# Performance work log

Hardware: AMD Instinct MI355X
Metric: run time of the kernel (lower is better)

## Reference

```python
import jax, jax.numpy as jnp
import numpy as np

D_MODEL = 1024
NUM_HEADS = 16
HEAD_DIM = D_MODEL // NUM_HEADS


def setup_inputs() -> dict:
    key = jax.random.key(0)
    ks = jax.random.split(key, 8)
    B, L, D = 4, 4096, D_MODEL
    s = 1.0 / np.sqrt(D)
    return {
        "x": jax.random.normal(ks[0], (B, L, D), dtype=jnp.float32),
        "y": jax.random.normal(ks[1], (B, L, D), dtype=jnp.float32),
        "Wkv": jax.random.normal(ks[2], (D, 2 * D), dtype=jnp.float32) * s,
        "bkv": jnp.zeros((2 * D,), dtype=jnp.float32),
        "Wq": jax.random.normal(ks[3], (D, D), dtype=jnp.float32) * s,
        "bq": jnp.zeros((D,), dtype=jnp.float32),
        "Wo": jax.random.normal(ks[4], (D, D), dtype=jnp.float32) * s,
        "bo": jnp.zeros((D,), dtype=jnp.float32),
    }


def reference(x, y, Wkv, bkv, Wq, bq, Wo, bo):
    B, L, D = x.shape
    H, hd = NUM_HEADS, HEAD_DIM
    # projections (torch Linear: x @ W^T + b; here W stored as [in,out])
    kv = (x @ Wkv + bkv).reshape(B, L, H, 2 * hd)
    q = (y @ Wq + bq).reshape(B, L, H, hd)
    # NOTE: source's permute() results are discarded, so attention is taken
    # over the HEADS axis at each position: attn shape [B, L, H, H].
    k, v = jnp.split(kv, 2, axis=-1)  # each [B, L, H, hd]
    scale = 1.0 / np.sqrt(hd)
    attn = jnp.einsum("blhd,blgd->blhg", q, k) * scale  # [B,L,H,H]
    attn = jax.nn.softmax(attn, axis=-1)
    val = jnp.einsum("blhg,blgd->blhd", attn, v).reshape(B, L, D)
    return val @ Wo + bo
```

## Files before the change

### kernel.cpp

```cpp
#include <hip/hip_runtime.h>
#include <math.h>


typedef __attribute__((ext_vector_type(8))) short bf16x8;
typedef __attribute__((ext_vector_type(4))) float f32x4;

__device__ __forceinline__ float b2f(short s) {
    union { unsigned u; float f; } x;
    x.u = ((unsigned)(unsigned short)s) << 16;
    return x.f;
}
__device__ __forceinline__ short f2b(float f) {
    union { float f; unsigned u; } x;
    x.f = f;
    unsigned r = (x.u + 0x7FFFu + ((x.u >> 16) & 1u)) >> 16;
    return (short)r;
}

__global__ __launch_bounds__(256) void cast2_f32_bf16(
    const float* __restrict__ in0, short* __restrict__ out0,
    const float* __restrict__ in1, short* __restrict__ out1, int n) {
    int i = (blockIdx.x * 256 + threadIdx.x) * 4;
    const float* in = in0;
    short* out = out0;
    if (i >= n) {
        i -= n;
        in = in1;
        out = out1;
    }
    float4 v = *(const float4*)(in + i);
    short4 o;
    o.x = f2b(v.x); o.y = f2b(v.y); o.z = f2b(v.z); o.w = f2b(v.w);
    *(short4*)(out + i) = o;
}

__global__ __launch_bounds__(256) void transpose_cast2(
    const float* __restrict__ W0, short* __restrict__ Wt0,
    const float* __restrict__ W1, short* __restrict__ Wt1, int K, int N) {
    const float* W = blockIdx.z ? W1 : W0;
    short* Wt = blockIdx.z ? Wt1 : Wt0;
    __shared__ float tile[32][33];
    int tx = threadIdx.x;
    int ty = threadIdx.y;
    int bx = blockIdx.x * 32;
    int by = blockIdx.y * 32;
#pragma unroll
    for (int j = 0; j < 32; j += 8)
        tile[ty + j][tx] = W[(size_t)(by + ty + j) * N + bx + tx];
    __syncthreads();
#pragma unroll
    for (int j = 0; j < 32; j += 8)
        Wt[(size_t)(bx + ty + j) * K + by + tx] = f2b(tile[tx][ty + j]);
}

#define BM 256
#define BN 256
#define BK 64

#define SUBOFF(c, ab, ks) (((((c) * 2 + (ab)) * 2 + (ks))) * 8192)

#define GLD16(g, l)                                           \
    __builtin_amdgcn_global_load_lds(                         \
        (const __attribute__((address_space(1))) void*)(g),   \
        (__attribute__((address_space(3))) void*)(l), 16, 0, 0)

#define STAGE_A(c, ks, kk)                                                   \
    do {                                                                     \
        GLD16(agp + (kk) + (ks) * 32, lbase + SUBOFF(c, 0, ks) * 2 + dst);   \
        GLD16(agp + (kk) + (ks) * 32 + qstep,                                \
              lbase + SUBOFF(c, 0, ks) * 2 + 8192 + dst);                    \
    } while (0)

#define STAGE_B(c, ks, kk)                                                   \
    do {                                                                     \
        GLD16(bgp + (kk) + (ks) * 32, lbase + SUBOFF(c, 1, ks) * 2 + dst);   \
        GLD16(bgp + (kk) + (ks) * 32 + qstep,                                \
              lbase + SUBOFF(c, 1, ks) * 2 + 8192 + dst);                    \
    } while (0)

#define MFMA_CLUSTER(MH)                                                     \
    do {                                                                     \
        asm volatile("s_waitcnt lgkmcnt(0)" ::: "memory");                   \
        __builtin_amdgcn_sched_barrier(0);                                   \
        __builtin_amdgcn_s_setprio(1);                                       \
        _Pragma("unroll") for (int i_ = 0; i_ < 4; ++i_)                     \
            _Pragma("unroll") for (int j_ = 0; j_ < 4; ++j_)                 \
                acc[(MH) + i_][j_] = __builtin_amdgcn_mfma_f32_16x16x32_bf16(\
                    af[i_], bf[j_], acc[(MH) + i_][j_], 0, 0, 0);            \
        __builtin_amdgcn_s_setprio(0);                                       \
    } while (0)

template <int OUT_BF16>
__global__ __launch_bounds__(512, 2) void gemm_bt(
    const short* __restrict__ A,
    const short* __restrict__ Bt,
    const float* __restrict__ bias,
    void* __restrict__ Cout,
    int M, int N, int K) {
    __shared__ __align__(16) short lds[65536];

    const int tid = threadIdx.x;

    const int NX = gridDim.x;
    const int nwg = NX * gridDim.y;
    int lin = blockIdx.y * NX + blockIdx.x;
    lin = (lin & 7) * (nwg >> 3) + (lin >> 3);
    const int bn = (lin % NX) * BN;
    const int bm = (lin / NX) * BM;

    const int lane = tid & 63;
    const int wave = tid >> 6;
    const int wr = wave >> 2;
    const int wc = wave & 3;
    const int fr = lane & 15;
    const int kq = lane >> 4;
    const int rsw = (kq ^ ((fr >> 1) & 3)) << 3;
    const int aro = (wr * 128 + fr) * 32 + rsw;
    const int bro = (wc * 64 + fr) * 32 + rsw;

    const int srow = tid >> 2;
    const int sslot = ((tid & 3) ^ ((tid >> 3) & 3)) * 8;
    const short* agp = A + (size_t)(bm + srow) * K + sslot;
    const short* bgp = Bt + (size_t)(bn + srow) * K + sslot;
    const size_t qstep = (size_t)128 * K;
    char* const lbase = (char*)lds;
    const int dst = tid * 16;

    f32x4 acc[8][4];
#pragma unroll
    for (int i = 0; i < 8; ++i)
#pragma unroll
        for (int j = 0; j < 4; ++j) acc[i][j] = (f32x4){0.f, 0.f, 0.f, 0.f};

    STAGE_A(0, 0, 0);
    STAGE_B(0, 0, 0);
    STAGE_A(0, 1, 0);
    STAGE_B(0, 1, 0);
    asm volatile("s_waitcnt vmcnt(4)" ::: "memory");
    __builtin_amdgcn_s_barrier();

    const int NT = K >> 6;
    for (int t = 0; t < NT; ++t) {
        const int c = t & 1, cn = c ^ 1;
        const int knext = (t + 1 < NT ? t + 1 : t) << 6;
        bf16x8 af[4], bf[4];
        const short* la0 = &lds[SUBOFF(c, 0, 0) + aro];
        const short* lb0 = &lds[SUBOFF(c, 1, 0) + bro];
#pragma unroll
        for (int i = 0; i < 4; ++i) af[i] = *(const bf16x8*)(la0 + i * 512);
#pragma unroll
        for (int j = 0; j < 4; ++j) bf[j] = *(const bf16x8*)(lb0 + j * 512);
        STAGE_A(cn, 0, knext);
        __builtin_amdgcn_sched_barrier(0);
        __builtin_amdgcn_s_barrier();
        MFMA_CLUSTER(0);
        __builtin_amdgcn_s_barrier();
#pragma unroll
        for (int i = 0; i < 4; ++i)
            af[i] = *(const bf16x8*)(la0 + (4 + i) * 512);
        STAGE_B(cn, 0, knext);
        __builtin_amdgcn_sched_barrier(0);
        __builtin_amdgcn_s_barrier();
        MFMA_CLUSTER(4);
        asm volatile("s_waitcnt vmcnt(4)" ::: "memory");
        __builtin_amdgcn_s_barrier();
        const short* la1 = &lds[SUBOFF(c, 0, 1) + aro];
        const short* lb1 = &lds[SUBOFF(c, 1, 1) + bro];
#pragma unroll
        for (int i = 0; i < 4; ++i) af[i] = *(const bf16x8*)(la1 + i * 512);
#pragma unroll
        for (int j = 0; j < 4; ++j) bf[j] = *(const bf16x8*)(lb1 + j * 512);
        STAGE_A(cn, 1, knext);
        __builtin_amdgcn_sched_barrier(0);
        __builtin_amdgcn_s_barrier();
        MFMA_CLUSTER(0);
        __builtin_amdgcn_s_barrier();
#pragma unroll
        for (int i = 0; i < 4; ++i)
            af[i] = *(const bf16x8*)(la1 + (4 + i) * 512);
        STAGE_B(cn, 1, knext);
        __builtin_amdgcn_sched_barrier(0);
        __builtin_amdgcn_s_barrier();
        MFMA_CLUSTER(4);
        asm volatile("s_waitcnt vmcnt(4)" ::: "memory");
        __builtin_amdgcn_s_barrier();
    }

#pragma unroll
    for (int ni = 0; ni < 4; ++ni) {
        const int col = bn + wc * 64 + ni * 16 + fr;
        const float bv = bias[col];
#pragma unroll
        for (int mi = 0; mi < 8; ++mi) {
            const int row0 = bm + wr * 128 + mi * 16 + kq * 4;
#pragma unroll
            for (int r = 0; r < 4; ++r) {
                float v = acc[mi][ni][r] + bv;
                if (OUT_BF16)
                    ((short*)Cout)[(size_t)(row0 + r) * N + col] = f2b(v);
                else
                    ((float*)Cout)[(size_t)(row0 + r) * N + col] = v;
            }
        }
    }
    asm volatile("s_waitcnt vmcnt(0)" ::: "memory");
}

__global__ __launch_bounds__(256) void attn_kernel(
    const short* __restrict__ Q, const short* __restrict__ KV,
    short* __restrict__ VAL) {
    const int wave = threadIdx.x >> 6;
    const int lane = threadIdx.x & 63;
    const size_t p = (size_t)blockIdx.x * 4 + wave;
    const int dq = lane & 3;

    const bf16x8* qp = (const bf16x8*)(Q + p * 1024 + (size_t)lane * 16);
    bf16x8 q0 = qp[0], q1 = qp[1];
    float q[16];
#pragma unroll
    for (int j = 0; j < 8; ++j) {
        q[j] = b2f(q0[j]);
        q[8 + j] = b2f(q1[j]);
    }

    const short* kvb = KV + p * 2048;

    float s[16];
#pragma unroll
    for (int g = 0; g < 16; ++g) {
        const bf16x8* kp = (const bf16x8*)(kvb + g * 128 + dq * 16);
        bf16x8 k0 = kp[0], k1 = kp[1];
        float d = 0.f;
#pragma unroll
        for (int j = 0; j < 8; ++j) {
            d += q[j] * b2f(k0[j]);
            d += q[8 + j] * b2f(k1[j]);
        }
        s[g] = d;
    }
    float mx = -1e30f;
#pragma unroll
    for (int g = 0; g < 16; ++g) {
        s[g] += __shfl_xor(s[g], 1, 64);
        s[g] += __shfl_xor(s[g], 2, 64);
        s[g] *= 0.125f;
        mx = fmaxf(mx, s[g]);
    }
    float ssum = 0.f;
#pragma unroll
    for (int g = 0; g < 16; ++g) {
        s[g] = __expf(s[g] - mx);
        ssum += s[g];
    }
    const float inv = 1.0f / ssum;

    float vo[16];
#pragma unroll
    for (int j = 0; j < 16; ++j) vo[j] = 0.f;
#pragma unroll
    for (int g = 0; g < 16; ++g) {
        const float w = s[g] * inv;
        const bf16x8* vp = (const bf16x8*)(kvb + g * 128 + 64 + dq * 16);
        bf16x8 v0 = vp[0], v1 = vp[1];
#pragma unroll
        for (int j = 0; j < 8; ++j) {
            vo[j] += w * b2f(v0[j]);
            vo[8 + j] += w * b2f(v1[j]);
        }
    }

    bf16x8 o0, o1;
#pragma unroll
    for (int j = 0; j < 8; ++j) {
        o0[j] = f2b(vo[j]);
        o1[j] = f2b(vo[8 + j]);
    }
    bf16x8* op = (bf16x8*)(VAL + p * 1024 + (size_t)lane * 16);
    op[0] = o0;
    op[1] = o1;
}

extern "C" void kernel_launch(void* const* d_in, const int* in_sizes, int n_in,
                              void* d_out, int out_size, void* d_ws,
                              size_t ws_size, hipStream_t stream) {
    const float* x = (const float*)d_in[0];
    const float* y = (const float*)d_in[1];
    const float* Wkv = (const float*)d_in[2];
    const float* bkv = (const float*)d_in[3];
    const float* Wq = (const float*)d_in[4];
    const float* bq = (const float*)d_in[5];
    const float* Wo = (const float*)d_in[6];
    const float* bo = (const float*)d_in[7];
    float* out = (float*)d_out;

    const int D = 1024;
    const int M = 16384;

    char* ws = (char*)d_ws;
    short* Xb = (short*)(ws);
    short* Yb = (short*)(ws + 33554432);
    short* Wkvt = (short*)(ws + 67108864);
    short* Wqt = (short*)(ws + 71303168);
    short* Wot = (short*)(ws + 73400320);
    short* KV = (short*)(ws + 75497472);
    short* Q = Xb;
    short* VAL = Yb;

    const int n = M * D;

    cast2_f32_bf16<<<2 * n / 1024, 256, 0, stream>>>(x, Xb, y, Yb, n);
    transpose_cast2<<<dim3(2 * D / 32, D / 32, 1), dim3(32, 8), 0, stream>>>(
        Wkv, Wkvt, (const float*)0, (short*)0, D, 2 * D);
    transpose_cast2<<<dim3(D / 32, D / 32, 2), dim3(32, 8), 0, stream>>>(
        Wq, Wqt, Wo, Wot, D, D);

    gemm_bt<1><<<dim3(2 * D / BN, M / BM), 512, 0, stream>>>(
        Xb, Wkvt, bkv, KV, M, 2 * D, D);
    gemm_bt<1><<<dim3(D / BN, M / BM), 512, 0, stream>>>(
        Yb, Wqt, bq, Q, M, D, D);
    attn_kernel<<<M / 4, 256, 0, stream>>>(Q, KV, VAL);
    gemm_bt<0><<<dim3(D / BN, M / BM), 512, 0, stream>>>(
        VAL, Wot, bo, out, M, D, D);
}
```

Measured before the change: 395.3 us.

## Replace double-buffered GEMM K-loop with four-slot ring buffer prefetching three stages ahead

Restructures the bf16 GEMM main loop from a two-buffer scheme with 64-wide K tiles into a four-slot LDS ring of 32-wide K sub-tiles, keeping three stages of global-to-LDS loads in flight. The goal is to hide more global memory latency behind the MFMA clusters. The epilogue is also reordered so bias values are loaded once and stores iterate over columns in the inner loop. The deeper pipeline uses the same 128KB of LDS but adds more outstanding loads per wave, and the loop assumes K/32 is a multiple of 4.

```diff
diff --git a/kernel.cpp b/kernel.cpp
--- a/kernel.cpp
+++ b/kernel.cpp
@@ -55,28 +55,11 @@
 
 #define BM 256
 #define BN 256
-#define BK 64
-
-#define SUBOFF(c, ab, ks) (((((c) * 2 + (ab)) * 2 + (ks))) * 8192)
 
 #define GLD16(g, l)                                           \
     __builtin_amdgcn_global_load_lds(                         \
         (const __attribute__((address_space(1))) void*)(g),   \
         (__attribute__((address_space(3))) void*)(l), 16, 0, 0)
-
-#define STAGE_A(c, ks, kk)                                                   \
-    do {                                                                     \
-        GLD16(agp + (kk) + (ks) * 32, lbase + SUBOFF(c, 0, ks) * 2 + dst);   \
-        GLD16(agp + (kk) + (ks) * 32 + qstep,                                \
-              lbase + SUBOFF(c, 0, ks) * 2 + 8192 + dst);                    \
-    } while (0)
-
-#define STAGE_B(c, ks, kk)                                                   \
-    do {                                                                     \
-        GLD16(bgp + (kk) + (ks) * 32, lbase + SUBOFF(c, 1, ks) * 2 + dst);   \
-        GLD16(bgp + (kk) + (ks) * 32 + qstep,                                \
-              lbase + SUBOFF(c, 1, ks) * 2 + 8192 + dst);                    \
-    } while (0)
 
 #define MFMA_CLUSTER(MH)                                                     \
     do {                                                                     \
@@ -86,7 +69,7 @@
         _Pragma("unroll") for (int i_ = 0; i_ < 4; ++i_)                     \
             _Pragma("unroll") for (int j_ = 0; j_ < 4; ++j_)                 \
                 acc[(MH) + i_][j_] = __builtin_amdgcn_mfma_f32_16x16x32_bf16(\
-                    af[i_], bf[j_], acc[(MH) + i_][j_], 0, 0, 0);            \
+                    af[i_], bfr[j_], acc[(MH) + i_][j_], 0, 0, 0);           \
         __builtin_amdgcn_s_setprio(0);                                       \
     } while (0)
 
@@ -132,74 +115,69 @@
 #pragma unroll
         for (int j = 0; j < 4; ++j) acc[i][j] = (f32x4){0.f, 0.f, 0.f, 0.f};
 
-    STAGE_A(0, 0, 0);
-    STAGE_B(0, 0, 0);
-    STAGE_A(0, 1, 0);
-    STAGE_B(0, 1, 0);
-    asm volatile("s_waitcnt vmcnt(4)" ::: "memory");
+#pragma unroll
+    for (int h = 0; h < 3; ++h) {
+        const int kk = h << 5;
+        GLD16(agp + kk, lbase + h * 32768 + dst);
+        GLD16(agp + kk + qstep, lbase + h * 32768 + 8192 + dst);
+        GLD16(bgp + kk, lbase + h * 32768 + 16384 + dst);
+        GLD16(bgp + kk + qstep, lbase + h * 32768 + 24576 + dst);
+    }
+    asm volatile("s_waitcnt vmcnt(8)" ::: "memory");
     __builtin_amdgcn_s_barrier();
 
-    const int NT = K >> 6;
-    for (int t = 0; t < NT; ++t) {
-        const int c = t & 1, cn = c ^ 1;
-        const int knext = (t + 1 < NT ? t + 1 : t) << 6;
-        bf16x8 af[4], bf[4];
-        const short* la0 = &lds[SUBOFF(c, 0, 0) + aro];
-        const short* lb0 = &lds[SUBOFF(c, 1, 0) + bro];
-#pragma unroll
-        for (int i = 0; i < 4; ++i) af[i] = *(const bf16x8*)(la0 + i * 512);
-#pragma unroll
-        for (int j = 0; j < 4; ++j) bf[j] = *(const bf16x8*)(lb0 + j * 512);
-        STAGE_A(cn, 0, knext);
-        __builtin_amdgcn_sched_barrier(0);
-        __builtin_amdgcn_s_barrier();
-        MFMA_CLUSTER(0);
-        __builtin_amdgcn_s_barrier();
-#pragma unroll
-        for (int i = 0; i < 4; ++i)
-            af[i] = *(const bf16x8*)(la0 + (4 + i) * 512);
-        STAGE_B(cn, 0, knext);
-        __builtin_amdgcn_sched_barrier(0);
-        __builtin_amdgcn_s_barrier();
-        MFMA_CLUSTER(4);
-        asm volatile("s_waitcnt vmcnt(4)" ::: "memory");
-        __builtin_amdgcn_s_barrier();
-        const short* la1 = &lds[SUBOFF(c, 0, 1) + aro];
-        const short* lb1 = &lds[SUBOFF(c, 1, 1) + bro];
-#pragma unroll
-        for (int i = 0; i < 4; ++i) af[i] = *(const bf16x8*)(la1 + i * 512);
-#pragma unroll
-        for (int j = 0; j < 4; ++j) bf[j] = *(const bf16x8*)(lb1 + j * 512);
-        STAGE_A(cn, 1, knext);
-        __builtin_amdgcn_sched_barrier(0);
-        __builtin_amdgcn_s_barrier();
-        MFMA_CLUSTER(0);
-        __builtin_amdgcn_s_barrier();
-#pragma unroll
-        for (int i = 0; i < 4; ++i)
-            af[i] = *(const bf16x8*)(la1 + (4 + i) * 512);
-        STAGE_B(cn, 1, knext);
-        __builtin_amdgcn_sched_barrier(0);
-        __builtin_amdgcn_s_barrier();
-        MFMA_CLUSTER(4);
-        asm volatile("s_waitcnt vmcnt(4)" ::: "memory");
-        __builtin_amdgcn_s_barrier();
-    }
-
-#pragma unroll
-    for (int ni = 0; ni < 4; ++ni) {
-        const int col = bn + wc * 64 + ni * 16 + fr;
-        const float bv = bias[col];
-#pragma unroll
-        for (int mi = 0; mi < 8; ++mi) {
-            const int row0 = bm + wr * 128 + mi * 16 + kq * 4;
-#pragma unroll
-            for (int r = 0; r < 4; ++r) {
-                float v = acc[mi][ni][r] + bv;
+    const int NH = K >> 5;
+    for (int mm = 0; mm < NH; mm += 4) {
+#pragma unroll
+        for (int u = 0; u < 4; ++u) {
+            const int m = mm + u;
+            const int slot = u;
+            const int wslot = (u + 3) & 3;
+            const int kis = ((m + 3 < NH) ? (m + 3) : (NH - 1)) << 5;
+            const short* la = &lds[slot * 16384 + aro];
+            const short* lb = &lds[slot * 16384 + 8192 + bro];
+            bf16x8 af[4], bfr[4];
+#pragma unroll
+            for (int i = 0; i < 4; ++i)
+                af[i] = *(const bf16x8*)(la + i * 512);
+#pragma unroll
+            for (int j = 0; j < 4; ++j)
+                bfr[j] = *(const bf16x8*)(lb + j * 512);
+            GLD16(agp + kis, lbase + wslot * 32768 + dst);
+            GLD16(agp + kis + qstep, lbase + wslot * 32768 + 8192 + dst);
+            __builtin_amdgcn_sched_barrier(0);
+            __builtin_amdgcn_s_barrier();
+            MFMA_CLUSTER(0);
+            __builtin_amdgcn_s_barrier();
+#pragma unroll
+            for (int i = 0; i < 4; ++i)
+                af[i] = *(const bf16x8*)(la + (4 + i) * 512);
+            GLD16(bgp + kis, lbase + wslot * 32768 + 16384 + dst);
+            GLD16(bgp + kis + qstep, lbase + wslot * 32768 + 24576 + dst);
+            __builtin_amdgcn_sched_barrier(0);
+            __builtin_amdgcn_s_barrier();
+            MFMA_CLUSTER(4);
+            asm volatile("s_waitcnt vmcnt(8)" ::: "memory");
+            __builtin_amdgcn_s_barrier();
+        }
+    }
+
+    float bvv[4];
+#pragma unroll
+    for (int ni = 0; ni < 4; ++ni) bvv[ni] = bias[bn + wc * 64 + ni * 16 + fr];
+#pragma unroll
+    for (int mi = 0; mi < 8; ++mi) {
+#pragma unroll
+        for (int r = 0; r < 4; ++r) {
+            const int row = bm + wr * 128 + mi * 16 + kq * 4 + r;
+#pragma unroll
+            for (int ni = 0; ni < 4; ++ni) {
+                const int col = bn + wc * 64 + ni * 16 + fr;
+                float v = acc[mi][ni][r] + bvv[ni];
                 if (OUT_BF16)
-                    ((short*)Cout)[(size_t)(row0 + r) * N + col] = f2b(v);
+                    ((short*)Cout)[(size_t)row * N + col] = f2b(v);
                 else
-                    ((float*)Cout)[(size_t)(row0 + r) * N + col] = v;
+                    ((float*)Cout)[(size_t)row * N + col] = v;
             }
         }
     }
```

Measured after the change: 373.6 us. 1.06x faster.
